# Kernel optimization log

Hardware: AMD Instinct MI355X
Metric: run time of the kernel (lower is better)

## Reference

```python
import jax, jax.numpy as jnp
import numpy as np

NEG_CLAMP = -100.0  # torch F.binary_cross_entropy clamps log terms at -100


def _ccl_labels(fg):
    """4-connectivity connected-component labeling of a [H,W] bool mask.
    Labels are assigned in raster-scan first-encounter order, matching
    scipy.ndimage.label with the default structure. Background = 0.
    Implemented as min-index label propagation to a fixed point: each
    component ends up tagged with the min flat index of its pixels (its
    first raster-scan pixel), then roots are ranked by cumsum to get 1..num.
    """
    H, W = fg.shape
    INF = H * W  # sentinel larger than any flat index
    idx = jnp.arange(INF, dtype=jnp.int32).reshape(H, W)
    init = jnp.where(fg, idx, INF)

    def step(x):
        up = jnp.concatenate([x[1:], jnp.full((1, W), INF, x.dtype)], axis=0)
        down = jnp.concatenate([jnp.full((1, W), INF, x.dtype), x[:-1]], axis=0)
        left = jnp.concatenate([x[:, 1:], jnp.full((H, 1), INF, x.dtype)], axis=1)
        right = jnp.concatenate([jnp.full((H, 1), INF, x.dtype), x[:, :-1]], axis=1)
        m = jnp.minimum(jnp.minimum(up, down), jnp.minimum(left, right))
        return jnp.where(fg, jnp.minimum(x, m), INF)

    def cond(carry):
        return carry[1]

    def body(carry):
        x, _ = carry
        nx = step(x)
        return nx, jnp.any(nx != x)

    x, _ = jax.lax.while_loop(cond, body, (init, jnp.array(True)))

    flat = x.reshape(-1)
    fgf = fg.reshape(-1)
    # a pixel is the root of its component iff its propagated tag == its own index
    is_root = fgf & (flat == jnp.arange(INF, dtype=jnp.int32))
    rank = jnp.cumsum(is_root.astype(jnp.int32))  # rank[r] = scipy label of root r
    labels = jnp.where(fgf, rank[jnp.clip(flat, 0, INF - 1)], 0)
    return labels.reshape(H, W)


def _target_map(fg):
    """Replicates: labels == labels.flatten()[1:].argmax() + 1 (faithful to source,
    including its quirky use of argmax position as the selected label value)."""
    labels = _ccl_labels(fg)
    lf = labels.reshape(-1)
    v = jnp.argmax(lf[1:]) + 1  # first occurrence of max, like numpy argmax
    return (labels == v).astype(jnp.float32)


def setup_inputs() -> dict:
    key = jax.random.key(0)
    pred = jax.random.uniform(key, (32, 1, 512, 512), dtype=jnp.float32)
    return {"pred": pred}


def reference(pred):
    fg = pred[:, 0] >= 0.5  # [N,H,W] bool
    target = jax.vmap(_target_map)(fg)[:, None]  # [N,1,H,W] float
    logp = jnp.maximum(jnp.log(pred), NEG_CLAMP)
    log1mp = jnp.maximum(jnp.log1p(-pred), NEG_CLAMP)
    return -jnp.mean(target * logp + (1.0 - target) * log1mp)
```

## Files before the change

kernel.cpp:

```cpp
#include <hip/hip_runtime.h>
#include <math.h>

#define IMG_W 512
#define IMG_H 512
#define HW (IMG_W * IMG_H)
#define LOGHW 18
#define NIMG 32
#define NTOT (NIMG * HW)
#define TILE 64
#define TPI 64
#define NTILE (NIMG * TPI)
#define CPI 64
#define NSCHUNK (NIMG * CPI)
#define EDGE_N (NTILE * 64)
#define NPAIR (NIMG * 112)

__device__ __forceinline__ void uf_unite(int* L, int a, int b) {
    while (true) {
        int p = ((volatile int*)L)[a];
        while (p != a) { a = p; p = ((volatile int*)L)[a]; }
        p = ((volatile int*)L)[b];
        while (p != b) { b = p; p = ((volatile int*)L)[b]; }
        if (a == b) return;
        if (a < b) { int t = a; a = b; b = t; }
        int old = atomicMin(&L[a], b);
        if (old == a) return;
        a = old;
    }
}

__global__ __launch_bounds__(512) void k_local(const float* __restrict__ pred,
                                               int* __restrict__ L,
                                               float* __restrict__ partials,
                                               int* __restrict__ edges,
                                               unsigned int* __restrict__ counter) {
    __shared__ int lab[TILE * TILE];
    __shared__ float sred[512];
    int tile = blockIdx.x;
    int img = tile >> 6;
    int t = tile & (TPI - 1);
    int ty = t >> 3, tx = t & 7;
    int baseLocal = (ty * TILE) * IMG_W + tx * TILE;
    const float* pi = pred + ((size_t)img << LOGHW);
    int* Li = L + ((size_t)img << LOGHW);
    int tid = threadIdx.x;
    int lane = tid & 63, wave = tid >> 6;

    float acc = 0.0f;
#pragma unroll
    for (int j = 0; j < 8; j++) {
        int row = wave + j * 8;
        float p = pi[baseLocal + row * IMG_W + lane];
        acc += fmaxf(__logf(1.0f - p), -100.0f);
        bool fg = (p >= 0.5f);
        unsigned long long bal = __ballot(fg);
        unsigned long long starts = bal & ~(bal << 1);
        unsigned long long maskle =
            (lane == 63) ? ~0ULL : ((1ULL << (lane + 1)) - 1ULL);
        int lb = -1;
        if (fg) {
            unsigned long long pre = starts & maskle;
            lb = row * TILE + (63 - __builtin_clzll(pre));
        }
        lab[row * TILE + lane] = lb;
    }
    __syncthreads();
#pragma unroll
    for (int j = 0; j < 8; j++) {
        int row = wave + j * 8;
        if (row == 0) continue;
        int i = row * TILE + lane;
        bool c = (lab[i] >= 0) && (lab[i - TILE] >= 0);
        unsigned long long cb = __ballot(c);
        unsigned long long cs = cb & ~(cb << 1);
        if ((cs >> lane) & 1ULL) uf_unite(lab, i, i - TILE);
    }
    __syncthreads();
#pragma unroll
    for (int j = 0; j < 8; j++) {
        int row = wave + j * 8;
        int i = row * TILE + lane;
        bool fg = (lab[i] >= 0);
        unsigned long long bal = __ballot(fg);
        unsigned long long st = bal & ~(bal << 1);
        if ((st >> lane) & 1ULL) {
            int x = i, p = lab[x];
            while (p != x) {
                int g = lab[p];
                lab[x] = g;
                x = g;
                p = lab[x];
            }
            lab[i] = x;
        }
    }
    __syncthreads();
#pragma unroll
    for (int j = 0; j < 2; j++) {
        int i4 = (tid + j * 512) * 4;
        int ly = i4 >> 6, lx = i4 & 63;
        int4 o;
        int* op = (int*)&o;
#pragma unroll
        for (int k = 0; k < 4; k++) {
            int s = lab[i4 + k];
            if (s < 0) op[k] = -1;
            else {
                int r = lab[s];
                op[k] = baseLocal + (r >> 6) * IMG_W + (r & 63);
            }
        }
        *(int4*)(Li + baseLocal + ly * IMG_W + lx) = o;
    }
    if (tid < 256) {
        int e = tid >> 6;
        int q = tid & 63;
        int px = (e == 0) ? q
               : (e == 1) ? (63 * TILE + q)
               : (e == 2) ? (q * TILE)
               :            (q * TILE + 63);
        int s = lab[px];
        int val = -1;
        if (s >= 0) {
            int r = lab[s];
            val = baseLocal + (r >> 6) * IMG_W + (r & 63);
        }
        edges[e * EDGE_N + tile * 64 + q] = val;
    }
    sred[tid] = acc;
    __syncthreads();
    for (int s = 256; s > 0; s >>= 1) {
        if (tid < s) sred[tid] += sred[tid + s];
        __syncthreads();
    }
    if (tid == 0) partials[blockIdx.x] = sred[0];
    if (blockIdx.x == 0 && tid == 0) *counter = 0u;
}

__global__ __launch_bounds__(256) void k_border(const int* __restrict__ edges,
                                                int* __restrict__ L) {
    int gid = blockIdx.x * blockDim.x + threadIdx.x;
    int pair = gid >> 6;
    int lane = gid & 63;
    int a, b, img;
    if (pair < NIMG * 56) {
        img = pair / 56;
        int w = pair - img * 56;
        int ty = w / 7, tx = w - ty * 7;
        int tl = img * TPI + ty * 8 + tx;
        a = edges[3 * EDGE_N + tl * 64 + lane];
        b = edges[2 * EDGE_N + (tl + 1) * 64 + lane];
    } else {
        int p2 = pair - NIMG * 56;
        img = p2 / 56;
        int w = p2 - img * 56;
        int ty = w >> 3, tx = w & 7;
        int tu = img * TPI + ty * 8 + tx;
        a = edges[1 * EDGE_N + tu * 64 + lane];
        b = edges[0 * EDGE_N + (tu + 8) * 64 + lane];
    }
    bool c = (a >= 0) && (b >= 0);
    unsigned long long cb = __ballot(c);
    unsigned long long cs = cb & ~(cb << 1);
    if ((cs >> lane) & 1ULL)
        uf_unite(L + ((size_t)img << LOGHW), a, b);
}

__global__ __launch_bounds__(256) void k_stats(const int* __restrict__ L,
                                               int* __restrict__ cntArr,
                                               int* __restrict__ maxArr,
                                               int* __restrict__ minArr) {
    __shared__ int s1[256], s2[256], s3[256];
    int chunk = blockIdx.x;
    int img = chunk >> 6;
    int baseL = (chunk & 63) * 4096;
    const int* Li = L + ((size_t)img << LOGHW);
    int t = threadIdx.x;
    int cnt = 0, mx = -1, mn = HW;
#pragma unroll
    for (int j = 0; j < 4; j++) {
        int off = baseL + (t + j * 256) * 4;
        int4 l4 = *(const int4*)(Li + off);
        const int* lp = (const int*)&l4;
#pragma unroll
        for (int k = 0; k < 4; k++) {
            int local = off + k;
            int p = lp[k];
            bool root = (p == local);
            cnt += root ? 1 : 0;
            if (root && local > mx) mx = local;
            if (p >= 0 && local >= 1 && local < mn) mn = local;
        }
    }
    s1[t] = cnt; s2[t] = mx; s3[t] = mn;
    __syncthreads();
    for (int s = 128; s > 0; s >>= 1) {
        if (t < s) {
            s1[t] += s1[t + s];
            s2[t] = max(s2[t], s2[t + s]);
            s3[t] = min(s3[t], s3[t + s]);
        }
        __syncthreads();
    }
    if (t == 0) { cntArr[chunk] = s1[0]; maxArr[chunk] = s2[0]; minArr[chunk] = s3[0]; }
}

__global__ __launch_bounds__(256) void k_tail(const int* __restrict__ cntArr,
                                              const int* __restrict__ maxArr,
                                              const int* __restrict__ minArr,
                                              const int* __restrict__ L,
                                              const float* __restrict__ pred,
                                              const float* __restrict__ partials,
                                              float* __restrict__ corr,
                                              unsigned int* __restrict__ counter,
                                              float* __restrict__ out) {
    __shared__ int sc[256], sm[256], sn[256];
    __shared__ int sel_chunk, sel_base, result;
    __shared__ float sf[256];
    __shared__ double sd[256];
    __shared__ unsigned int oldc;
    int img = blockIdx.x, t = threadIdx.x;
    const int* Li = L + ((size_t)img << LOGHW);
    int cnt = (t < CPI) ? cntArr[img * CPI + t] : 0;
    sc[t] = cnt;
    sm[t] = (t < CPI) ? maxArr[img * CPI + t] : -1;
    sn[t] = (t < CPI) ? minArr[img * CPI + t] : HW;
    if (t == 0) result = -2;
    __syncthreads();
    for (int off = 1; off < 256; off <<= 1) {
        int v2 = (t >= off) ? sc[t - off] : 0;
        __syncthreads();
        sc[t] += v2;
        __syncthreads();
    }
    int num = sc[255];
    int inc = sc[t], exc = inc - cnt;
    for (int s = 128; s > 0; s >>= 1) {
        if (t < s) { sm[t] = max(sm[t], sm[t + s]); sn[t] = min(sn[t], sn[t + s]); }
        __syncthreads();
    }
    int last_root = sm[0], minFg = sn[0];
    int v;
    if (last_root >= 1) v = last_root;
    else if (last_root == 0) v = (minFg < HW) ? minFg : 1;
    else v = 1;
    if (v >= 1 && v <= num) {
        if (exc < v && v <= inc) { sel_chunk = t; sel_base = exc; }
        __syncthreads();
        int c = sel_chunk, base = sel_base;
        int baseL = c * 4096;
        int f[16];
        int sum = 0;
#pragma unroll
        for (int j = 0; j < 4; j++) {
            int off = baseL + t * 16 + j * 4;
            int4 l4 = *(const int4*)(Li + off);
            const int* lp = (const int*)&l4;
#pragma unroll
            for (int k = 0; k < 4; k++) {
                f[j * 4 + k] = (lp[k] == off + k) ? 1 : 0;
                sum += f[j * 4 + k];
            }
        }
        __syncthreads();
        sc[t] = sum;
        __syncthreads();
        for (int off = 1; off < 256; off <<= 1) {
            int v2 = (t >= off) ? sc[t - off] : 0;
            __syncthreads();
            sc[t] += v2;
            __syncthreads();
        }
        int exc2 = sc[t] - sum;
        int need = v - base;
        if (exc2 < need && need <= sc[t]) {
            int run = exc2;
#pragma unroll
            for (int k = 0; k < 16; k++) {
                run += f[k];
                if (run == need) { result = baseL + t * 16 + k; break; }
            }
        }
        __syncthreads();
    } else {
        __syncthreads();
    }
    int rvv = result;
    float blocksum = 0.0f;
    if (rvv >= 0) {
        const float* pi = pred + ((size_t)img << LOGHW);
        float acc = 0.0f;
        for (int it = 0; it < HW / 1024; it++) {
            int off = it * 1024 + t * 4;
            float4 p4 = *(const float4*)(pi + off);
            int4 l4 = *(const int4*)(Li + off);
            const float* pp = (const float*)&p4;
            const int* lp = (const int*)&l4;
#pragma unroll
            for (int k = 0; k < 4; k++) {
                int p = lp[k];
                if (p < 0) continue;
                int x = p, q = Li[x];
                while (q != x) { x = q; q = Li[x]; }
                if (x == rvv) {
                    float pr = pp[k];
                    acc += fmaxf(__logf(pr), -100.0f)
                         - fmaxf(__logf(1.0f - pr), -100.0f);
                }
            }
        }
        sf[t] = acc;
        __syncthreads();
        for (int s = 128; s > 0; s >>= 1) {
            if (t < s) sf[t] += sf[t + s];
            __syncthreads();
        }
        blocksum = sf[0];
    }
    if (t == 0) {
        __hip_atomic_store(&corr[img], blocksum, __ATOMIC_RELAXED,
                           __HIP_MEMORY_SCOPE_AGENT);
        oldc = __hip_atomic_fetch_add(counter, 1u, __ATOMIC_ACQ_REL,
                                      __HIP_MEMORY_SCOPE_AGENT);
    }
    __syncthreads();
    if (oldc != NIMG - 1) return;
    double acc = 0.0;
#pragma unroll
    for (int j = 0; j < 8; j++) acc += (double)partials[t + j * 256];
    if (t < NIMG)
        acc += (double)__hip_atomic_load(&corr[t], __ATOMIC_ACQUIRE,
                                         __HIP_MEMORY_SCOPE_AGENT);
    sd[t] = acc;
    __syncthreads();
    for (int s = 128; s > 0; s >>= 1) {
        if (t < s) sd[t] += sd[t + s];
        __syncthreads();
    }
    if (t == 0) out[0] = (float)(-sd[0] / (double)NTOT);
}

extern "C" void kernel_launch(void* const* d_in, const int* in_sizes, int n_in,
                              void* d_out, int out_size, void* d_ws, size_t ws_size,
                              hipStream_t stream) {
    const float* pred = (const float*)d_in[0];
    float* out = (float*)d_out;

    char* ws = (char*)d_ws;
    int* L = (int*)ws;
    int* edges = (int*)(ws + (size_t)NTOT * 4);
    int* cntArr = edges + 4 * EDGE_N;
    int* maxArr = cntArr + NSCHUNK;
    int* minArr = maxArr + NSCHUNK;
    float* partials = (float*)(minArr + NSCHUNK);
    float* corr = partials + NTILE;
    unsigned int* counter = (unsigned int*)(corr + NIMG);

    k_local<<<dim3(NTILE), dim3(512), 0, stream>>>(pred, L, partials, edges, counter);
    k_border<<<dim3(NPAIR * 64 / 256), dim3(256), 0, stream>>>(edges, L);
    k_stats<<<dim3(NSCHUNK), dim3(256), 0, stream>>>(L, cntArr, maxArr, minArr);
    k_tail<<<dim3(NIMG), dim3(256), 0, stream>>>(cntArr, maxArr, minArr, L, pred,
                                                 partials, corr, counter, out);
}
```

Baseline: 121.0 us.

## Drop k_stats pass by emitting per-tile root lists from local labeling

Result: slower. 163.4 us (+35.0%).

```diff
diff --git a/kernel.cpp b/kernel.cpp
--- a/kernel.cpp
+++ b/kernel.cpp
@@ -10,10 +10,9 @@
 #define TILE 64
 #define TPI 64
 #define NTILE (NIMG * TPI)
-#define CPI 64
-#define NSCHUNK (NIMG * CPI)
 #define EDGE_N (NTILE * 64)
 #define NPAIR (NIMG * 112)
+#define RTSTRIDE 2048
 
 __device__ __forceinline__ void uf_unite(int* L, int a, int b) {
     while (true) {
@@ -33,9 +32,14 @@
                                                int* __restrict__ L,
                                                float* __restrict__ partials,
                                                int* __restrict__ edges,
+                                               int* __restrict__ rootCnt,
+                                               int* __restrict__ rootList,
+                                               unsigned int* __restrict__ minFgT,
                                                unsigned int* __restrict__ counter) {
     __shared__ int lab[TILE * TILE];
-    __shared__ float sred[512];
+    __shared__ float swf[8];
+    __shared__ unsigned swu[8];
+    __shared__ int rootc;
     int tile = blockIdx.x;
     int img = tile >> 6;
     int t = tile & (TPI - 1);
@@ -45,14 +49,18 @@
     int* Li = L + ((size_t)img << LOGHW);
     int tid = threadIdx.x;
     int lane = tid & 63, wave = tid >> 6;
+    if (tid == 0) rootc = 0;
 
     float acc = 0.0f;
+    unsigned umn = 0xFFFFFFFFu;
 #pragma unroll
     for (int j = 0; j < 8; j++) {
         int row = wave + j * 8;
-        float p = pi[baseLocal + row * IMG_W + lane];
+        int fl = baseLocal + row * IMG_W + lane;
+        float p = pi[fl];
         acc += fmaxf(__logf(1.0f - p), -100.0f);
         bool fg = (p >= 0.5f);
+        if (fg && fl != 0) umn = min(umn, (unsigned)fl);
         unsigned long long bal = __ballot(fg);
         unsigned long long starts = bal & ~(bal << 1);
         unsigned long long maskle =
@@ -95,22 +103,32 @@
         }
     }
     __syncthreads();
+    int* rl = rootList + (size_t)tile * RTSTRIDE;
 #pragma unroll
     for (int j = 0; j < 2; j++) {
         int i4 = (tid + j * 512) * 4;
-        int ly = i4 >> 6, lx = i4 & 63;
+        int4 s4 = *(const int4*)&lab[i4];
+        const int* sp = (const int*)&s4;
         int4 o;
         int* op = (int*)&o;
+        int rc = 0;
 #pragma unroll
         for (int k = 0; k < 4; k++) {
-            int s = lab[i4 + k];
+            int s = sp[k];
             if (s < 0) op[k] = -1;
             else {
                 int r = lab[s];
                 op[k] = baseLocal + (r >> 6) * IMG_W + (r & 63);
+                if (s == i4 + k) rc++;
             }
         }
-        *(int4*)(Li + baseLocal + ly * IMG_W + lx) = o;
+        *(int4*)(Li + baseLocal + (i4 >> 6) * IMG_W + (i4 & 63)) = o;
+        if (rc) {
+            int base = atomicAdd(&rootc, rc);
+#pragma unroll
+            for (int k = 0; k < 4; k++)
+                if (sp[k] == i4 + k) rl[base++] = op[k];
+        }
     }
     if (tid < 256) {
         int e = tid >> 6;
@@ -127,14 +145,22 @@
         }
         edges[e * EDGE_N + tile * 64 + q] = val;
     }
-    sred[tid] = acc;
-    __syncthreads();
-    for (int s = 256; s > 0; s >>= 1) {
-        if (tid < s) sred[tid] += sred[tid + s];
-        __syncthreads();
-    }
-    if (tid == 0) partials[blockIdx.x] = sred[0];
-    if (blockIdx.x == 0 && tid == 0) *counter = 0u;
+#pragma unroll
+    for (int o = 32; o > 0; o >>= 1) {
+        acc += __shfl_down(acc, o);
+        umn = min(umn, (unsigned)__shfl_down((int)umn, o));
+    }
+    if (lane == 0) { swf[wave] = acc; swu[wave] = umn; }
+    __syncthreads();
+    if (tid == 0) {
+        float s = 0.0f; unsigned m = 0xFFFFFFFFu;
+#pragma unroll
+        for (int w = 0; w < 8; w++) { s += swf[w]; m = min(m, swu[w]); }
+        partials[blockIdx.x] = s;
+        rootCnt[tile] = rootc;
+        minFgT[tile] = m;
+        if (blockIdx.x == 0) *counter = 0u;
+    }
 }
 
 __global__ __launch_bounds__(256) void k_border(const int* __restrict__ edges,
@@ -166,104 +192,91 @@
         uf_unite(L + ((size_t)img << LOGHW), a, b);
 }
 
-__global__ __launch_bounds__(256) void k_stats(const int* __restrict__ L,
-                                               int* __restrict__ cntArr,
-                                               int* __restrict__ maxArr,
-                                               int* __restrict__ minArr) {
-    __shared__ int s1[256], s2[256], s3[256];
-    int chunk = blockIdx.x;
-    int img = chunk >> 6;
-    int baseL = (chunk & 63) * 4096;
-    const int* Li = L + ((size_t)img << LOGHW);
-    int t = threadIdx.x;
-    int cnt = 0, mx = -1, mn = HW;
-#pragma unroll
-    for (int j = 0; j < 4; j++) {
-        int off = baseL + (t + j * 256) * 4;
-        int4 l4 = *(const int4*)(Li + off);
-        const int* lp = (const int*)&l4;
-#pragma unroll
-        for (int k = 0; k < 4; k++) {
-            int local = off + k;
-            int p = lp[k];
-            bool root = (p == local);
-            cnt += root ? 1 : 0;
-            if (root && local > mx) mx = local;
-            if (p >= 0 && local >= 1 && local < mn) mn = local;
-        }
-    }
-    s1[t] = cnt; s2[t] = mx; s3[t] = mn;
-    __syncthreads();
-    for (int s = 128; s > 0; s >>= 1) {
-        if (t < s) {
-            s1[t] += s1[t + s];
-            s2[t] = max(s2[t], s2[t + s]);
-            s3[t] = min(s3[t], s3[t + s]);
-        }
-        __syncthreads();
-    }
-    if (t == 0) { cntArr[chunk] = s1[0]; maxArr[chunk] = s2[0]; minArr[chunk] = s3[0]; }
-}
-
-__global__ __launch_bounds__(256) void k_tail(const int* __restrict__ cntArr,
-                                              const int* __restrict__ maxArr,
-                                              const int* __restrict__ minArr,
+__global__ __launch_bounds__(256) void k_tail(const int* __restrict__ rootCnt,
+                                              const int* __restrict__ rootList,
+                                              const unsigned int* __restrict__ minFgT,
                                               const int* __restrict__ L,
                                               const float* __restrict__ pred,
                                               const float* __restrict__ partials,
                                               float* __restrict__ corr,
                                               unsigned int* __restrict__ counter,
                                               float* __restrict__ out) {
+    __shared__ int pre[65];
     __shared__ int sc[256], sm[256], sn[256];
-    __shared__ int sel_chunk, sel_base, result;
+    __shared__ int result;
     __shared__ float sf[256];
     __shared__ double sd[256];
     __shared__ unsigned int oldc;
     int img = blockIdx.x, t = threadIdx.x;
     const int* Li = L + ((size_t)img << LOGHW);
-    int cnt = (t < CPI) ? cntArr[img * CPI + t] : 0;
-    sc[t] = cnt;
-    sm[t] = (t < CPI) ? maxArr[img * CPI + t] : -1;
-    sn[t] = (t < CPI) ? minArr[img * CPI + t] : HW;
+
+    if (t < 64) {
+        int v = rootCnt[img * TPI + t];
+#pragma unroll
+        for (int o = 1; o < 64; o <<= 1) {
+            int u = __shfl_up(v, o);
+            if (t >= o) v += u;
+        }
+        pre[t + 1] = v;
+        if (t == 0) pre[0] = 0;
+    }
     if (t == 0) result = -2;
     __syncthreads();
-    for (int off = 1; off < 256; off <<= 1) {
-        int v2 = (t >= off) ? sc[t - off] : 0;
-        __syncthreads();
-        sc[t] += v2;
-        __syncthreads();
-    }
-    int num = sc[255];
-    int inc = sc[t], exc = inc - cnt;
+    int C = pre[64];
+
+    int cnt = 0, mx = -1;
+    for (int k0 = t; k0 < C; k0 += 2048) {
+        int rr0 = -1, rr1 = -1, rr2 = -1, rr3 = -1,
+            rr4 = -1, rr5 = -1, rr6 = -1, rr7 = -1;
+#define PROBE(J, RR)                                                        \
+        {                                                                   \
+            int k = k0 + (J) * 256;                                         \
+            if (k < C) {                                                    \
+                int lo = 0, hi = 64;                                        \
+                for (int s = 0; s < 6; s++) {                               \
+                    int mid = (lo + hi) >> 1;                               \
+                    if (pre[mid] <= k) lo = mid; else hi = mid;             \
+                }                                                           \
+                RR = rootList[(size_t)(img * TPI + lo) * RTSTRIDE           \
+                              + (k - pre[lo])];                             \
+            }                                                               \
+        }
+        PROBE(0, rr0) PROBE(1, rr1) PROBE(2, rr2) PROBE(3, rr3)
+        PROBE(4, rr4) PROBE(5, rr5) PROBE(6, rr6) PROBE(7, rr7)
+#undef PROBE
+#define TEST(RR) if ((RR) >= 0 && Li[RR] == (RR)) { cnt++; mx = max(mx, RR); }
+        TEST(rr0) TEST(rr1) TEST(rr2) TEST(rr3)
+        TEST(rr4) TEST(rr5) TEST(rr6) TEST(rr7)
+#undef TEST
+    }
+    unsigned mnu = (t < 64) ? minFgT[img * TPI + t] : 0xFFFFFFFFu;
+    sc[t] = cnt; sm[t] = mx;
+    sn[t] = (int)min(mnu, (unsigned)HW);
+    __syncthreads();
     for (int s = 128; s > 0; s >>= 1) {
-        if (t < s) { sm[t] = max(sm[t], sm[t + s]); sn[t] = min(sn[t], sn[t + s]); }
-        __syncthreads();
-    }
-    int last_root = sm[0], minFg = sn[0];
+        if (t < s) {
+            sc[t] += sc[t + s];
+            sm[t] = max(sm[t], sm[t + s]);
+            sn[t] = min(sn[t], sn[t + s]);
+        }
+        __syncthreads();
+    }
+    int num = sc[0], last_root = sm[0], minFg = sn[0];
     int v;
     if (last_root >= 1) v = last_root;
     else if (last_root == 0) v = (minFg < HW) ? minFg : 1;
     else v = 1;
+
     if (v >= 1 && v <= num) {
-        if (exc < v && v <= inc) { sel_chunk = t; sel_base = exc; }
-        __syncthreads();
-        int c = sel_chunk, base = sel_base;
-        int baseL = c * 4096;
-        int f[16];
-        int sum = 0;
-#pragma unroll
-        for (int j = 0; j < 4; j++) {
-            int off = baseL + t * 16 + j * 4;
+        int base = t * (HW / 256);
+        int c = 0;
+        for (int j = 0; j < 256; j++) {
+            int off = base + j * 4;
             int4 l4 = *(const int4*)(Li + off);
-            const int* lp = (const int*)&l4;
-#pragma unroll
-            for (int k = 0; k < 4; k++) {
-                f[j * 4 + k] = (lp[k] == off + k) ? 1 : 0;
-                sum += f[j * 4 + k];
-            }
-        }
-        __syncthreads();
-        sc[t] = sum;
+            c += (l4.x == off) + (l4.y == off + 1)
+               + (l4.z == off + 2) + (l4.w == off + 3);
+        }
+        sc[t] = c;
         __syncthreads();
         for (int off = 1; off < 256; off <<= 1) {
             int v2 = (t >= off) ? sc[t - off] : 0;
@@ -271,18 +284,19 @@
             sc[t] += v2;
             __syncthreads();
         }
-        int exc2 = sc[t] - sum;
-        int need = v - base;
-        if (exc2 < need && need <= sc[t]) {
-            int run = exc2;
-#pragma unroll
-            for (int k = 0; k < 16; k++) {
-                run += f[k];
-                if (run == need) { result = baseL + t * 16 + k; break; }
+        int inc = sc[t], exc = inc - c;
+        if (exc < v && v <= inc) {
+            int need = v - exc, run = 0;
+            for (int j = 0; j < 256; j++) {
+                int off = base + j * 4;
+                int4 l4 = *(const int4*)(Li + off);
+                if (l4.x == off)     { run++; if (run == need) result = off; }
+                if (l4.y == off + 1) { run++; if (run == need) result = off + 1; }
+                if (l4.z == off + 2) { run++; if (run == need) result = off + 2; }
+                if (l4.w == off + 3) { run++; if (run == need) result = off + 3; }
+                if (run >= need) break;
             }
         }
-        __syncthreads();
-    } else {
         __syncthreads();
     }
     int rvv = result;
@@ -349,16 +363,18 @@
     char* ws = (char*)d_ws;
     int* L = (int*)ws;
     int* edges = (int*)(ws + (size_t)NTOT * 4);
-    int* cntArr = edges + 4 * EDGE_N;
-    int* maxArr = cntArr + NSCHUNK;
-    int* minArr = maxArr + NSCHUNK;
-    float* partials = (float*)(minArr + NSCHUNK);
+    int* rootList = edges + 4 * EDGE_N;
+    int* rootCnt = rootList + (size_t)NTILE * RTSTRIDE;
+    unsigned int* minFgT = (unsigned int*)(rootCnt + NTILE);
+    float* partials = (float*)(minFgT + NTILE);
     float* corr = partials + NTILE;
     unsigned int* counter = (unsigned int*)(corr + NIMG);
 
-    k_local<<<dim3(NTILE), dim3(512), 0, stream>>>(pred, L, partials, edges, counter);
+    k_local<<<dim3(NTILE), dim3(512), 0, stream>>>(pred, L, partials, edges,
+                                                   rootCnt, rootList, minFgT,
+                                                   counter);
     k_border<<<dim3(NPAIR * 64 / 256), dim3(256), 0, stream>>>(edges, L);
-    k_stats<<<dim3(NSCHUNK), dim3(256), 0, stream>>>(L, cntArr, maxArr, minArr);
-    k_tail<<<dim3(NIMG), dim3(256), 0, stream>>>(cntArr, maxArr, minArr, L, pred,
-                                                 partials, corr, counter, out);
-}
+    k_tail<<<dim3(NIMG), dim3(256), 0, stream>>>(rootCnt, rootList, minFgT, L,
+                                                 pred, partials, corr, counter,
+                                                 out);
+}
```
